# Kernel tuning notes

Hardware: AMD Instinct MI355X
Metric: run time of the kernel (lower is better)

## Reference

```python
import jax, jax.numpy as jnp
from jax import lax
import numpy as np


def _relu(x):
    return jnp.maximum(x, 0)


def setup_inputs() -> dict:
    key = jax.random.key(0)
    ks = jax.random.split(key, 20)
    B = 1024
    s = 0.05  # small init scale
    d = {
        "raw_input": jax.random.normal(ks[0], (B, 1, 28, 28), jnp.float32),
        "output_embed": jax.random.normal(ks[1], (B, 512), jnp.float32),
        "latent_embed": jax.random.normal(ks[2], (B, 512), jnp.float32),
        "conv1_w": jax.random.normal(ks[3], (16, 1, 3, 3), jnp.float32) * s,
        "conv1_b": jax.random.normal(ks[4], (16,), jnp.float32) * s,
        "conv2_w": jax.random.normal(ks[5], (32, 16, 3, 3), jnp.float32) * s,
        "conv2_b": jax.random.normal(ks[6], (32,), jnp.float32) * s,
        "proj_w1": jax.random.normal(ks[7], (1568, 1024), jnp.float32) * s,
        "proj_b1": jax.random.normal(ks[8], (1024,), jnp.float32) * s,
        "proj_w2": jax.random.normal(ks[9], (1024, 512), jnp.float32) * s,
        "proj_b2": jax.random.normal(ks[10], (512,), jnp.float32) * s,
        "bb_w1": jax.random.normal(ks[11], (512, 1024), jnp.float32) * s,
        "bb_b1": jax.random.normal(ks[12], (1024,), jnp.float32) * s,
        "bb_w2": jax.random.normal(ks[13], (1024, 512), jnp.float32) * s,
        "bb_b2": jax.random.normal(ks[14], (512,), jnp.float32) * s,
        "head_w": jax.random.normal(ks[15], (512, 10), jnp.float32) * s,
        "head_b": jax.random.normal(ks[16], (10,), jnp.float32) * s,
        "Nsup": 16,
        "n_latent": 6,
    }
    return d


def _maxpool2(x):
    # 2x2 max pool, stride 2, NCHW
    return lax.reduce_window(x, -jnp.inf, lax.max, (1, 1, 2, 2), (1, 1, 2, 2), "VALID")


def reference(raw_input, output_embed, latent_embed,
              conv1_w, conv1_b, conv2_w, conv2_b,
              proj_w1, proj_b1, proj_w2, proj_b2,
              bb_w1, bb_b1, bb_w2, bb_b2,
              head_w, head_b, Nsup, n_latent):
    dn = ("NCHW", "OIHW", "NCHW")
    B = raw_input.shape[0]

    def backbone(x):
        return _relu(_relu(x @ bb_w1 + bb_b1) @ bb_w2 + bb_b2)

    def latent_recursion(inp, out, lat, n):
        if n > 0:
            for _ in range(n):
                lat = backbone(inp + out + lat)
            out = backbone(lat + inp)
        else:
            out = backbone(inp + out + lat)
        return out, lat

    # CNN extractor + input embedding projection (B, 512)
    x = _relu(lax.conv_general_dilated(raw_input, conv1_w, (1, 1), "SAME",
                                       dimension_numbers=dn) + conv1_b[None, :, None, None])
    x = _maxpool2(x)  # (B,16,14,14)
    x = _relu(lax.conv_general_dilated(x, conv2_w, (1, 1), "SAME",
                                       dimension_numbers=dn) + conv2_b[None, :, None, None])
    x = _maxpool2(x)  # (B,32,7,7)
    h = x.reshape(B, -1)  # (B, 1568)
    inp = _relu(_relu(h @ proj_w1 + proj_b1) @ proj_w2 + proj_b2)  # (B,512)

    sg = lax.stop_gradient
    out, lat = output_embed, latent_embed
    T = 3
    logits = None
    for _ in range(Nsup):
        # deep_recursion: T-1 no-grad latent recursions, then one tracked
        for _ in range(T - 1):
            out, lat = latent_recursion(inp, out, lat, n_latent)
            out, lat = sg(out), sg(lat)
        out, lat = latent_recursion(inp, out, lat, n_latent)
        logits = out @ head_w + head_b
        out, lat = sg(out), sg(lat)
    return logits
```

## Files before the change

kernel.cpp:

```cpp
#include <hip/hip_runtime.h>
#include <hip/hip_bf16.h>


typedef unsigned short ushort_t;
typedef __attribute__((ext_vector_type(8))) short short8;
typedef __attribute__((ext_vector_type(4))) float f32x4;

__device__ inline unsigned f2bf_rne(float v) {
    unsigned u = __float_as_uint(v);
    return (u + 0x7fffu + ((u >> 16) & 1u)) >> 16;
}
__device__ inline void split2(float v, ushort_t& h, ushort_t& l) {
    unsigned uh = f2bf_rne(v);
    h = (ushort_t)uh;
    float fh = __uint_as_float(uh << 16);
    l = (ushort_t)f2bf_rne(v - fh);
}

__global__ __launch_bounds__(256) void conv1_pool(
    const float* __restrict__ in, const float* __restrict__ w,
    const float* __restrict__ bias, float* __restrict__ out)
{
    int idx = blockIdx.x * 256 + threadIdx.x;
    int xo = idx % 14; int t = idx / 14;
    int yo = t % 14;  t /= 14;
    int oc = t % 16;  int b = t / 16;
    const float* ip = in + (size_t)b * 784;
    const float* wp = w + oc * 9;
    float win[4][4];
#pragma unroll
    for (int yy = 0; yy < 4; ++yy)
#pragma unroll
        for (int xx = 0; xx < 4; ++xx) {
            int y = 2 * yo + yy - 1, x = 2 * xo + xx - 1;
            win[yy][xx] = (y >= 0 && y < 28 && x >= 0 && x < 28) ? ip[y * 28 + x] : 0.f;
        }
    float bs = bias[oc];
    float m = -1e30f;
#pragma unroll
    for (int py = 0; py < 2; ++py)
#pragma unroll
        for (int px = 0; px < 2; ++px) {
            float s = bs;
#pragma unroll
            for (int dy = 0; dy < 3; ++dy)
#pragma unroll
                for (int dx = 0; dx < 3; ++dx)
                    s = fmaf(win[py + dy][px + dx], wp[dy * 3 + dx], s);
            m = fmaxf(m, s);
        }
    out[idx] = fmaxf(m, 0.f);
}

__global__ __launch_bounds__(256) void conv2_pool(
    const float* __restrict__ in, const float* __restrict__ w,
    const float* __restrict__ bias, float* __restrict__ out)
{
    __shared__ float ws_[32 * 16 * 9];
    for (int i = threadIdx.x; i < 4608; i += 256) ws_[i] = w[i];
    __syncthreads();
    int idx = blockIdx.x * 256 + threadIdx.x;
    int xo = idx % 7; int t = idx / 7;
    int yo = t % 7;  t /= 7;
    int oc = t % 32; int b = t / 32;
    const float* ip = in + (size_t)b * 16 * 196;
    float bs = bias[oc];
    float s00 = bs, s01 = bs, s10 = bs, s11 = bs;
    for (int ic = 0; ic < 16; ++ic) {
        const float* ipp = ip + ic * 196;
        float win[4][4];
#pragma unroll
        for (int yy = 0; yy < 4; ++yy)
#pragma unroll
            for (int xx = 0; xx < 4; ++xx) {
                int y = 2 * yo + yy - 1, x = 2 * xo + xx - 1;
                win[yy][xx] = (y >= 0 && y < 14 && x >= 0 && x < 14) ? ipp[y * 14 + x] : 0.f;
            }
        const float* wp = ws_ + (oc * 16 + ic) * 9;
#pragma unroll
        for (int dy = 0; dy < 3; ++dy)
#pragma unroll
            for (int dx = 0; dx < 3; ++dx) {
                float wv = wp[dy * 3 + dx];
                s00 = fmaf(win[0 + dy][0 + dx], wv, s00);
                s01 = fmaf(win[0 + dy][1 + dx], wv, s01);
                s10 = fmaf(win[1 + dy][0 + dx], wv, s10);
                s11 = fmaf(win[1 + dy][1 + dx], wv, s11);
            }
    }
    float m = fmaxf(fmaxf(s00, s01), fmaxf(s10, s11));
    out[idx] = fmaxf(m, 0.f);
}

#define BMF 64
#define BNF 64
#define BKF 16

__global__ __launch_bounds__(256) void gemm_f32(
    const float* __restrict__ A0, const float* __restrict__ W,
    const float* __restrict__ bias, float* __restrict__ C,
    int M, int N, int K)
{
    __shared__ float As[BKF][BMF];
    __shared__ float Bs[BKF][BNF];
    const int tid = threadIdx.x;
    const int tx = tid % 16;
    const int ty = tid / 16;
    const int row0 = blockIdx.y * BMF;
    const int col0 = blockIdx.x * BNF;
    float acc[4][4] = {};
    const int ra = tid / 4;
    const int ca = 4 * (tid % 4);
    const int rb = tid / 16;
    const int cb = 4 * (tid % 16);
    for (int k0 = 0; k0 < K; k0 += BKF) {
        float4 v = *(const float4*)(A0 + (size_t)(row0 + ra) * K + k0 + ca);
        float4 bvec = *(const float4*)(W + (size_t)(k0 + rb) * N + col0 + cb);
        As[ca + 0][ra] = v.x;
        As[ca + 1][ra] = v.y;
        As[ca + 2][ra] = v.z;
        As[ca + 3][ra] = v.w;
        *(float4*)&Bs[rb][cb] = bvec;
        __syncthreads();
#pragma unroll
        for (int kk = 0; kk < BKF; ++kk) {
            float4 av = *(const float4*)&As[kk][ty * 4];
            float4 bv = *(const float4*)&Bs[kk][tx * 4];
            float a_[4] = {av.x, av.y, av.z, av.w};
            float b_[4] = {bv.x, bv.y, bv.z, bv.w};
#pragma unroll
            for (int i = 0; i < 4; ++i)
#pragma unroll
                for (int j = 0; j < 4; ++j)
                    acc[i][j] = fmaf(a_[i], b_[j], acc[i][j]);
        }
        __syncthreads();
    }
    float4 bv = *(const float4*)(bias + col0 + tx * 4);
    float bb[4] = {bv.x, bv.y, bv.z, bv.w};
#pragma unroll
    for (int i = 0; i < 4; ++i) {
        float4 o;
        o.x = fmaxf(acc[i][0] + bb[0], 0.f);
        o.y = fmaxf(acc[i][1] + bb[1], 0.f);
        o.z = fmaxf(acc[i][2] + bb[2], 0.f);
        o.w = fmaxf(acc[i][3] + bb[3], 0.f);
        *(float4*)(C + (size_t)(row0 + ty * 4 + i) * N + col0 + tx * 4) = o;
    }
}

__global__ __launch_bounds__(256) void prep_wt(
    const float* __restrict__ w, ushort_t* __restrict__ th,
    ushort_t* __restrict__ tl, int K, int N)
{
    int idx = blockIdx.x * 256 + threadIdx.x;
    int n = idx / K, k = idx % K;
    float v = w[(size_t)k * N + n];
    split2(v, th[idx], tl[idx]);
}

__global__ __launch_bounds__(256) void init_xs(
    const float* __restrict__ inpf, const float* __restrict__ oute,
    const float* __restrict__ late, float* __restrict__ io,
    ushort_t* __restrict__ xh, ushort_t* __restrict__ xl)
{
    int i = blockIdx.x * 256 + threadIdx.x;
    float t = inpf[i] + oute[i];
    io[i] = t;
    split2(t + late[i], xh[i], xl[i]);
}

__global__ void init_bar(unsigned* bar) {
    bar[threadIdx.x] = 0;
    bar[threadIdx.x + 256] = 0;
}

__device__ __forceinline__ void group_barrier(unsigned* bar, int g,
                                              unsigned& tgt)
{
    __syncthreads();
    if (threadIdx.x == 0) {
        __builtin_amdgcn_fence(__ATOMIC_RELEASE, "workgroup");
        __hip_atomic_fetch_add(bar + g * 32, 1u, __ATOMIC_RELAXED,
                               __HIP_MEMORY_SCOPE_AGENT);
        while (__hip_atomic_load(bar + g * 32, __ATOMIC_RELAXED,
                                 __HIP_MEMORY_SCOPE_AGENT) < tgt)
            __builtin_amdgcn_s_sleep(1);
        __builtin_amdgcn_fence(__ATOMIC_ACQUIRE, "workgroup");
        asm volatile("buffer_inv sc0" ::: "memory");
    }
    tgt += 32;
    __syncthreads();
}

__device__ __forceinline__ short8 afrag(const ushort_t* __restrict__ p,
                                        int row, int K, int kpos)
{
    return *(const short8*)(p + (size_t)row * K + kpos);
}

__global__ __launch_bounds__(512, 2) void trm_persist(
    ushort_t* __restrict__ xs_hi, ushort_t* __restrict__ xs_lo,
    ushort_t* __restrict__ h1_hi, ushort_t* __restrict__ h1_lo,
    const ushort_t* __restrict__ W1h, const ushort_t* __restrict__ W1l,
    const ushort_t* __restrict__ W2h, const ushort_t* __restrict__ W2l,
    const float* __restrict__ bb1, const float* __restrict__ bb2,
    float* __restrict__ io, const float* __restrict__ inpf,
    float* __restrict__ latf, float* __restrict__ outf,
    const float* __restrict__ hw, const float* __restrict__ hb,
    float* __restrict__ logits, unsigned* bar)
{
    __shared__ __align__(16) unsigned char w1lds[65536];
    __shared__ __align__(16) unsigned char w2lds[65536];
    __shared__ int sh_gs;

    const int tid = threadIdx.x;
    const int w = tid >> 6, lane = tid & 63;
    const int q = lane >> 4, li = lane & 15;

    if (tid == 0) {
        unsigned xcc;
        asm volatile("s_getreg_b32 %0, hwreg(HW_REG_XCC_ID)" : "=s"(xcc));
        xcc &= 7u;
        unsigned s = __hip_atomic_fetch_add(bar + 384 + xcc * 8, 1u,
                                            __ATOMIC_RELAXED,
                                            __HIP_MEMORY_SCOPE_AGENT);
        sh_gs = (int)((xcc << 8) | (s & 31u));
    }
    __syncthreads();
    const int g = sh_gs >> 8;
    const int slot = sh_gs & 255;
    const int c1 = slot * 32;
    const int c2 = slot * 16;
    const int rowA = g * 128 + w * 16;

    for (int i = tid; i < 4096; i += 512) {
        int comp = i >> 11;
        int rem = i & 2047;
        int n = rem >> 6, c = rem & 63;
        const ushort_t* src = (comp ? W1l : W1h) + (size_t)(c1 + n) * 512 + c * 8;
        int dst = ((((comp << 4) + (c >> 2)) * 2 + (n >> 4)) * 64 +
                   ((c & 3) * 16 + (n & 15))) * 16;
        *(uint4*)(w1lds + dst) = *(const uint4*)src;
    }
    for (int i = tid; i < 4096; i += 512) {
        int comp = i >> 11;
        int rem = i & 2047;
        int n = rem >> 7, c = rem & 127;
        const ushort_t* src = (comp ? W2l : W2h) + (size_t)(c2 + n) * 1024 + c * 8;
        int dst = (((comp << 5) + (c >> 2)) * 64 + ((c & 3) * 16 + n)) * 16;
        *(uint4*)(w2lds + dst) = *(const uint4*)src;
    }
    __syncthreads();

    float bias1[2];
    bias1[0] = bb1[c1 + li];
    bias1[1] = bb1[c1 + 16 + li];
    float bias2 = bb2[c2 + li];
    unsigned tgt = 32;

    for (int step = 0; step < 336; ++step) {
        {
            f32x4 acc0 = {}, acc1 = {};
            short8 aF[4][2];
#pragma unroll
            for (int p = 0; p < 4; ++p) {
                int kp = p * 32 + q * 8;
                aF[p][0] = afrag(xs_hi, rowA + li, 512, kp);
                aF[p][1] = afrag(xs_lo, rowA + li, 512, kp);
            }
#pragma unroll
            for (int s = 0; s < 16; ++s) {
                short8 ah = aF[s & 3][0], al = aF[s & 3][1];
                if (s + 4 < 16) {
                    int kp = (s + 4) * 32 + q * 8;
                    aF[(s + 4) & 3][0] = afrag(xs_hi, rowA + li, 512, kp);
                    aF[(s + 4) & 3][1] = afrag(xs_lo, rowA + li, 512, kp);
                }
                const int base = (s * 2 * 64 + lane) * 16;
                short8 bh0 = *(const short8*)(w1lds + base);
                short8 bh1 = *(const short8*)(w1lds + base + 1024);
                short8 bl0 = *(const short8*)(w1lds + 32768 + base);
                short8 bl1 = *(const short8*)(w1lds + 32768 + base + 1024);
                acc0 = __builtin_amdgcn_mfma_f32_16x16x32_bf16(ah, bh0, acc0, 0, 0, 0);
                acc0 = __builtin_amdgcn_mfma_f32_16x16x32_bf16(ah, bl0, acc0, 0, 0, 0);
                acc0 = __builtin_amdgcn_mfma_f32_16x16x32_bf16(al, bh0, acc0, 0, 0, 0);
                acc0 = __builtin_amdgcn_mfma_f32_16x16x32_bf16(al, bl0, acc0, 0, 0, 0);
                acc1 = __builtin_amdgcn_mfma_f32_16x16x32_bf16(ah, bh1, acc1, 0, 0, 0);
                acc1 = __builtin_amdgcn_mfma_f32_16x16x32_bf16(ah, bl1, acc1, 0, 0, 0);
                acc1 = __builtin_amdgcn_mfma_f32_16x16x32_bf16(al, bh1, acc1, 0, 0, 0);
                acc1 = __builtin_amdgcn_mfma_f32_16x16x32_bf16(al, bl1, acc1, 0, 0, 0);
            }
#pragma unroll
            for (int tj = 0; tj < 2; ++tj) {
                int colg = c1 + tj * 16 + li;
                float bv = bias1[tj];
#pragma unroll
                for (int rr = 0; rr < 4; ++rr) {
                    int rowg = rowA + q * 4 + rr;
                    size_t idx = (size_t)rowg * 1024 + colg;
                    float v = fmaxf((tj ? acc1[rr] : acc0[rr]) + bv, 0.f);
                    split2(v, h1_hi[idx], h1_lo[idx]);
                }
            }
        }
        group_barrier(bar, g, tgt);

        {
            int im = step % 7;
            int mode = (im < 5) ? 1 : ((im == 5) ? 2 : 3);
            f32x4 acc = {};
            short8 aF[4][2];
#pragma unroll
            for (int p = 0; p < 4; ++p) {
                int kp = p * 32 + q * 8;
                aF[p][0] = afrag(h1_hi, rowA + li, 1024, kp);
                aF[p][1] = afrag(h1_lo, rowA + li, 1024, kp);
            }
#pragma unroll
            for (int s = 0; s < 32; ++s) {
                short8 ah = aF[s & 3][0], al = aF[s & 3][1];
                if (s + 4 < 32) {
                    int kp = (s + 4) * 32 + q * 8;
                    aF[(s + 4) & 3][0] = afrag(h1_hi, rowA + li, 1024, kp);
                    aF[(s + 4) & 3][1] = afrag(h1_lo, rowA + li, 1024, kp);
                }
                const int base = (s * 64 + lane) * 16;
                short8 bh = *(const short8*)(w2lds + base);
                short8 bl = *(const short8*)(w2lds + 32768 + base);
                acc = __builtin_amdgcn_mfma_f32_16x16x32_bf16(ah, bh, acc, 0, 0, 0);
                acc = __builtin_amdgcn_mfma_f32_16x16x32_bf16(ah, bl, acc, 0, 0, 0);
                acc = __builtin_amdgcn_mfma_f32_16x16x32_bf16(al, bh, acc, 0, 0, 0);
                acc = __builtin_amdgcn_mfma_f32_16x16x32_bf16(al, bl, acc, 0, 0, 0);
            }
            int colg = c2 + li;
#pragma unroll
            for (int rr = 0; rr < 4; ++rr) {
                int rowg = rowA + q * 4 + rr;
                size_t idx = (size_t)rowg * 512 + colg;
                float v = fmaxf(acc[rr] + bias2, 0.f);
                if (mode == 1) {
                    split2(io[idx] + v, xs_hi[idx], xs_lo[idx]);
                } else if (mode == 2) {
                    split2(inpf[idx] + v, xs_hi[idx], xs_lo[idx]);
                    latf[idx] = v;
                } else {
                    outf[idx] = v;
                    float t2 = inpf[idx] + v;
                    io[idx] = t2;
                    split2(t2 + latf[idx], xs_hi[idx], xs_lo[idx]);
                }
            }
        }
        group_barrier(bar, g, tgt);
    }

    {
        int idx = slot * 512 + tid;
        if (idx < 1280) {
            int rloc = idx / 10, j = idx % 10;
            int row = g * 128 + rloc;
            const float* r = outf + (size_t)row * 512;
            float s = hb[j];
            for (int k = 0; k < 512; ++k) s = fmaf(r[k], hw[k * 10 + j], s);
            logits[row * 10 + j] = s;
        }
    }
}

extern "C" void kernel_launch(void* const* d_in, const int* in_sizes, int n_in,
                              void* d_out, int out_size, void* d_ws, size_t ws_size,
                              hipStream_t stream)
{
    const float* raw   = (const float*)d_in[0];
    const float* out_e = (const float*)d_in[1];
    const float* lat_e = (const float*)d_in[2];
    const float* c1w = (const float*)d_in[3];
    const float* c1b = (const float*)d_in[4];
    const float* c2w = (const float*)d_in[5];
    const float* c2b = (const float*)d_in[6];
    const float* pw1 = (const float*)d_in[7];
    const float* pb1 = (const float*)d_in[8];
    const float* pw2 = (const float*)d_in[9];
    const float* pb2 = (const float*)d_in[10];
    const float* bw1 = (const float*)d_in[11];
    const float* bb1 = (const float*)d_in[12];
    const float* bw2 = (const float*)d_in[13];
    const float* bb2 = (const float*)d_in[14];
    const float* hw  = (const float*)d_in[15];
    const float* hb  = (const float*)d_in[16];

    char* base = (char*)d_ws;
    float*    pool1  = (float*)   (base + 0);
    ushort_t* h1_hi  = (ushort_t*)(base + 0);
    ushort_t* h1_lo  = (ushort_t*)(base + 2097152);
    ushort_t* xs_hi  = (ushort_t*)(base + 4194304);
    ushort_t* xs_lo  = (ushort_t*)(base + 5242880);
    float*    io     = (float*)   (base + 6291456);
    float*    latf   = (float*)   (base + 8388608);
    float*    h1f    = (float*)   (base + 0);
    float*    h      = (float*)   (base + 12845056);
    float*    inpf   = (float*)   (base + 19267584);
    float*    outf   = (float*)   (base + 21364736);
    ushort_t* bW1t_h = (ushort_t*)(base + 23461888);
    ushort_t* bW1t_l = (ushort_t*)(base + 24510464);
    ushort_t* bW2t_h = (ushort_t*)(base + 25559040);
    ushort_t* bW2t_l = (ushort_t*)(base + 26607616);
    unsigned* bar    = (unsigned*)(base + 27656192);

    prep_wt<<<2048, 256, 0, stream>>>(bw1, bW1t_h, bW1t_l, 512, 1024);
    prep_wt<<<2048, 256, 0, stream>>>(bw2, bW2t_h, bW2t_l, 1024, 512);
    init_bar<<<1, 256, 0, stream>>>(bar);

    conv1_pool<<<3211264 / 256, 256, 0, stream>>>(raw, c1w, c1b, pool1);
    conv2_pool<<<1605632 / 256, 256, 0, stream>>>(pool1, c2w, c2b, h);
    gemm_f32<<<dim3(16, 16), 256, 0, stream>>>(h, pw1, pb1, h1f, 1024, 1024, 1568);
    gemm_f32<<<dim3(8, 16), 256, 0, stream>>>(h1f, pw2, pb2, inpf, 1024, 512, 1024);
    init_xs<<<2048, 256, 0, stream>>>(inpf, out_e, lat_e, io, xs_hi, xs_lo);

    trm_persist<<<256, 512, 0, stream>>>(
        xs_hi, xs_lo, h1_hi, h1_lo, bW1t_h, bW1t_l, bW2t_h, bW2t_l,
        bb1, bb2, io, inpf, latf, outf, hw, hb, (float*)d_out, bar);
}
```

Baseline: 8.394 ms.

## Replace workgroup-wide group barrier with per-wave cross-block barriers and deepen prefetch

The block-level barrier, which used __syncthreads plus one atomic counter per 32-block group, is replaced by one counter per (group, wave) pair. Each wave now waits only on the 32 waves in other blocks that produce the same 16-row slice it consumes next. This drops the two __syncthreads per half-step and lets waves in a block run at different paces. The A-fragment prefetch ring grows from 4 to 8 stages in both GEMMs, at the cost of more registers. A final group-wide barrier is added before the logits head, and barrier init moves just before the persistent kernel to clear the new counter array.

```diff
diff --git a/kernel.cpp b/kernel.cpp
--- a/kernel.cpp
+++ b/kernel.cpp
@@ -170,27 +170,26 @@
     split2(t + late[i], xh[i], xl[i]);
 }
 
-__global__ void init_bar(unsigned* bar) {
+__global__ void init_bar(unsigned* bar, unsigned* wbar) {
     bar[threadIdx.x] = 0;
     bar[threadIdx.x + 256] = 0;
-}
-
-__device__ __forceinline__ void group_barrier(unsigned* bar, int g,
-                                              unsigned& tgt)
-{
-    __syncthreads();
-    if (threadIdx.x == 0) {
+    for (int i = threadIdx.x; i < 2048; i += 256) wbar[i] = 0;
+}
+
+__device__ __forceinline__ void wave_barrier(unsigned* ctr, unsigned& tgt,
+                                             int lane)
+{
+    if (lane == 0) {
         __builtin_amdgcn_fence(__ATOMIC_RELEASE, "workgroup");
-        __hip_atomic_fetch_add(bar + g * 32, 1u, __ATOMIC_RELAXED,
+        __hip_atomic_fetch_add(ctr, 1u, __ATOMIC_RELAXED,
                                __HIP_MEMORY_SCOPE_AGENT);
-        while (__hip_atomic_load(bar + g * 32, __ATOMIC_RELAXED,
+        while (__hip_atomic_load(ctr, __ATOMIC_RELAXED,
                                  __HIP_MEMORY_SCOPE_AGENT) < tgt)
             __builtin_amdgcn_s_sleep(1);
-        __builtin_amdgcn_fence(__ATOMIC_ACQUIRE, "workgroup");
-        asm volatile("buffer_inv sc0" ::: "memory");
-    }
+    }
+    __builtin_amdgcn_fence(__ATOMIC_ACQUIRE, "workgroup");
+    asm volatile("buffer_inv sc0" ::: "memory");
     tgt += 32;
-    __syncthreads();
 }
 
 __device__ __forceinline__ short8 afrag(const ushort_t* __restrict__ p,
@@ -208,7 +207,7 @@
     float* __restrict__ io, const float* __restrict__ inpf,
     float* __restrict__ latf, float* __restrict__ outf,
     const float* __restrict__ hw, const float* __restrict__ hb,
-    float* __restrict__ logits, unsigned* bar)
+    float* __restrict__ logits, unsigned* bar, unsigned* wbar)
 {
     __shared__ __align__(16) unsigned char w1lds[65536];
     __shared__ __align__(16) unsigned char w2lds[65536];
@@ -233,6 +232,7 @@
     const int c1 = slot * 32;
     const int c2 = slot * 16;
     const int rowA = g * 128 + w * 16;
+    unsigned* wctr = wbar + (g * 8 + w) * 32;
 
     for (int i = tid; i < 4096; i += 512) {
         int comp = i >> 11;
@@ -262,20 +262,20 @@
     for (int step = 0; step < 336; ++step) {
         {
             f32x4 acc0 = {}, acc1 = {};
-            short8 aF[4][2];
-#pragma unroll
-            for (int p = 0; p < 4; ++p) {
+            short8 aF[8][2];
+#pragma unroll
+            for (int p = 0; p < 8; ++p) {
                 int kp = p * 32 + q * 8;
                 aF[p][0] = afrag(xs_hi, rowA + li, 512, kp);
                 aF[p][1] = afrag(xs_lo, rowA + li, 512, kp);
             }
 #pragma unroll
             for (int s = 0; s < 16; ++s) {
-                short8 ah = aF[s & 3][0], al = aF[s & 3][1];
-                if (s + 4 < 16) {
-                    int kp = (s + 4) * 32 + q * 8;
-                    aF[(s + 4) & 3][0] = afrag(xs_hi, rowA + li, 512, kp);
-                    aF[(s + 4) & 3][1] = afrag(xs_lo, rowA + li, 512, kp);
+                short8 ah = aF[s & 7][0], al = aF[s & 7][1];
+                if (s + 8 < 16) {
+                    int kp = (s + 8) * 32 + q * 8;
+                    aF[(s + 8) & 7][0] = afrag(xs_hi, rowA + li, 512, kp);
+                    aF[(s + 8) & 7][1] = afrag(xs_lo, rowA + li, 512, kp);
                 }
                 const int base = (s * 2 * 64 + lane) * 16;
                 short8 bh0 = *(const short8*)(w1lds + base);
@@ -304,26 +304,26 @@
                 }
             }
         }
-        group_barrier(bar, g, tgt);
+        wave_barrier(wctr, tgt, lane);
 
         {
             int im = step % 7;
             int mode = (im < 5) ? 1 : ((im == 5) ? 2 : 3);
             f32x4 acc = {};
-            short8 aF[4][2];
-#pragma unroll
-            for (int p = 0; p < 4; ++p) {
+            short8 aF[8][2];
+#pragma unroll
+            for (int p = 0; p < 8; ++p) {
                 int kp = p * 32 + q * 8;
                 aF[p][0] = afrag(h1_hi, rowA + li, 1024, kp);
                 aF[p][1] = afrag(h1_lo, rowA + li, 1024, kp);
             }
 #pragma unroll
             for (int s = 0; s < 32; ++s) {
-                short8 ah = aF[s & 3][0], al = aF[s & 3][1];
-                if (s + 4 < 32) {
-                    int kp = (s + 4) * 32 + q * 8;
-                    aF[(s + 4) & 3][0] = afrag(h1_hi, rowA + li, 1024, kp);
-                    aF[(s + 4) & 3][1] = afrag(h1_lo, rowA + li, 1024, kp);
+                short8 ah = aF[s & 7][0], al = aF[s & 7][1];
+                if (s + 8 < 32) {
+                    int kp = (s + 8) * 32 + q * 8;
+                    aF[(s + 8) & 7][0] = afrag(h1_hi, rowA + li, 1024, kp);
+                    aF[(s + 8) & 7][1] = afrag(h1_lo, rowA + li, 1024, kp);
                 }
                 const int base = (s * 64 + lane) * 16;
                 short8 bh = *(const short8*)(w2lds + base);
@@ -352,8 +352,19 @@
                 }
             }
         }
-        group_barrier(bar, g, tgt);
-    }
+        wave_barrier(wctr, tgt, lane);
+    }
+
+    if (lane == 0) {
+        __builtin_amdgcn_fence(__ATOMIC_RELEASE, "workgroup");
+        __hip_atomic_fetch_add(bar + g * 32, 1u, __ATOMIC_RELAXED,
+                               __HIP_MEMORY_SCOPE_AGENT);
+        while (__hip_atomic_load(bar + g * 32, __ATOMIC_RELAXED,
+                                 __HIP_MEMORY_SCOPE_AGENT) < 256u)
+            __builtin_amdgcn_s_sleep(1);
+    }
+    __builtin_amdgcn_fence(__ATOMIC_ACQUIRE, "workgroup");
+    asm volatile("buffer_inv sc0" ::: "memory");
 
     {
         int idx = slot * 512 + tid;
@@ -398,6 +409,7 @@
     ushort_t* xs_lo  = (ushort_t*)(base + 5242880);
     float*    io     = (float*)   (base + 6291456);
     float*    latf   = (float*)   (base + 8388608);
+    unsigned* wbar   = (unsigned*)(base + 10485760);
     float*    h1f    = (float*)   (base + 0);
     float*    h      = (float*)   (base + 12845056);
     float*    inpf   = (float*)   (base + 19267584);
@@ -410,7 +422,6 @@
 
     prep_wt<<<2048, 256, 0, stream>>>(bw1, bW1t_h, bW1t_l, 512, 1024);
     prep_wt<<<2048, 256, 0, stream>>>(bw2, bW2t_h, bW2t_l, 1024, 512);
-    init_bar<<<1, 256, 0, stream>>>(bar);
 
     conv1_pool<<<3211264 / 256, 256, 0, stream>>>(raw, c1w, c1b, pool1);
     conv2_pool<<<1605632 / 256, 256, 0, stream>>>(pool1, c2w, c2b, h);
@@ -418,7 +429,9 @@
     gemm_f32<<<dim3(8, 16), 256, 0, stream>>>(h1f, pw2, pb2, inpf, 1024, 512, 1024);
     init_xs<<<2048, 256, 0, stream>>>(inpf, out_e, lat_e, io, xs_hi, xs_lo);
 
+    init_bar<<<1, 256, 0, stream>>>(bar, wbar);
+
     trm_persist<<<256, 512, 0, stream>>>(
         xs_hi, xs_lo, h1_hi, h1_lo, bW1t_h, bW1t_l, bW2t_h, bW2t_l,
-        bb1, bb2, io, inpf, latf, outf, hw, hb, (float*)d_out, bar);
-}
+        bb1, bb2, io, inpf, latf, outf, hw, hb, (float*)d_out, bar, wbar);
+}
```

After: 22.97 ms. +173.7%, slower.
